# Kernel optimization log

Measured on AMD Instinct MI355X. Metric: run time of the kernel, lower is better.

Reference implementation:

```python
import jax, jax.numpy as jnp
import numpy as np

P = 16  # patch size
D = 768  # embedding dim


def setup_inputs() -> dict:
    key = jax.random.key(0)
    k_img, k_w, k_b = jax.random.split(key, 3)
    B, H, W, C = 64, 224, 224, 3
    image = jax.random.normal(k_img, (B, H, W, C), dtype=jnp.float32)
    patch_dim = P * P * C  # 768
    # Keras Dense default: glorot_uniform kernel, zeros bias
    limit = np.sqrt(6.0 / (patch_dim + D)).astype(np.float32)
    W_proj = jax.random.uniform(k_w, (patch_dim, D), dtype=jnp.float32,
                                minval=-limit, maxval=limit)
    b_proj = jnp.zeros((D,), dtype=jnp.float32)
    return {"image": image, "W_proj": W_proj, "b_proj": b_proj}


def reference(image, W_proj, b_proj):
    B, H, W, C = image.shape
    nh, nw = H // P, W // P
    # Fused im2col replacing the per-patch slicing loop:
    # [B,H,W,C] -> [B, nh, P, nw, P, C] -> [B, nh, nw, P, P, C] -> [B, nh*nw, P*P*C]
    # Row-major (p_i, p_j) patch order matches the original nested loop, and
    # flatten of a [B,P,P,C] slice matches the (P,P,C) raveling here.
    patches = image.reshape(B, nh, P, nw, P, C)
    patches = patches.transpose(0, 1, 3, 2, 4, 5).reshape(B, nh * nw, P * P * C)
    # Dense + exact GELU (tf.keras.activations.gelu default approximate=False)
    x = jnp.einsum('bnp,pd->bnd', patches, W_proj) + b_proj
    return jax.nn.gelu(x, approximate=False)
```

## Files before the change

kernel.cpp:

```cpp
#include <hip/hip_runtime.h>
#include <hip/hip_bf16.h>
#include <math.h>

#define MM 12544
#define KK 768
#define NN 768
#define BM 64
#define BN 128
#define BK 64
#define KT 12
#define MT 196
#define NT 6
#define TILE_B_BYTES (BN*BK*2)

#define WTPACK_BLOCKS ((NN * 96) / 256)

typedef __bf16 v8bf __attribute__((ext_vector_type(8)));
typedef float  v4f  __attribute__((ext_vector_type(4)));

__global__ __launch_bounds__(256) void wt_pack(const float* __restrict__ w,
                                               __hip_bfloat16* __restrict__ wpack) {
    int tid = blockIdx.x * 256 + threadIdx.x;
    int n   = tid % 768;
    int gg  = tid / 768;
    int k0  = gg * 8;
    float f[8];
#pragma unroll
    for (int j = 0; j < 8; j++) f[j] = w[(size_t)(k0 + j) * NN + n];
    int nt = n >> 7;
    int nr = n & 127;
    int kt = gg >> 3;
    int g  = gg & 7;
    int gs = g ^ (nr & 7);
    union { __hip_bfloat16 h[8]; uint4 u; } o;
#pragma unroll
    for (int j = 0; j < 8; j++) o.h[j] = __float2bfloat16(f[j]);
    *(uint4*)(wpack + ((size_t)(nt * KT + kt) * BN + nr) * BK + gs * 8) = o.u;
}

__device__ __forceinline__ float gelu_fast(float x) {
    float t2 = 1.5957691216057308f * x * (1.0f + 0.044715f * x * x);
    float e  = __expf(t2);
    float r  = __builtin_amdgcn_rcpf(e + 1.0f);
    return x - x * r;
}

__global__ __launch_bounds__(256, 5) void gemm_gelu(const float* __restrict__ img,
                                                    const __hip_bfloat16* __restrict__ wpack,
                                                    const float* __restrict__ bias,
                                                    float* __restrict__ out) {
    __shared__ __align__(16) __hip_bfloat16 As[BM * BK];
    __shared__ __align__(16) __hip_bfloat16 Bs[BN * BK];

    const int blk = blockIdx.x;
    const int nt  = blk % NT;
    const int mt  = blk / NT;

    const int tid  = threadIdx.x;
    const int lane = tid & 63;
    const int wave = tid >> 6;
    const int wn   = wave * 32;
    const int col  = lane & 15;
    const int quad = lane >> 4;
    const int cl7  = col & 7;

    const int r = tid >> 2;
    const int q = tid & 3;
    unsigned m  = (unsigned)(mt * BM + r);
    unsigned b  = m / 196u;
    unsigned pm = m - b * 196u;
    unsigned pr = pm / 14u;
    unsigned pc = pm - pr * 14u;
    const float* pbase = img + (size_t)(((b * 224u + pr * 16u) * 224u + pc * 16u) * 3u);
    const int gs0 = (2 * q) ^ (r & 7);
    const int gs1 = gs0 ^ 1;
    uint4* As16 = (uint4*)As;

    v4f acc[4][2];
    const v4f vzero = {0.f, 0.f, 0.f, 0.f};
#pragma unroll
    for (int a = 0; a < 4; a++)
#pragma unroll
        for (int c = 0; c < 2; c++) acc[a][c] = vzero;

    const char* bT = (const char*)wpack + (size_t)nt * KT * TILE_B_BYTES;

    for (int kt = 0; kt < KT; kt++) {
#pragma unroll
        for (int p = 0; p < 4; p++) {
            int off = p * 4096 + tid * 16;
            __builtin_amdgcn_global_load_lds(
                (const __attribute__((address_space(1))) void*)(bT + off),
                (__attribute__((address_space(3))) void*)((char*)Bs + off), 16, 0, 0);
        }
        bT += TILE_B_BYTES;

        float4 f4[4];
#pragma unroll
        for (int j = 0; j < 4; j++) {
            unsigned k   = (unsigned)(kt * 64 + q * 16 + j * 4);
            unsigned i   = k / 48u;
            unsigned rem = k - i * 48u;
            f4[j] = *(const float4*)(pbase + i * 672u + rem);
        }
        union { __hip_bfloat16 h[8]; uint4 u; } lo, hi;
        lo.h[0] = __float2bfloat16(f4[0].x); lo.h[1] = __float2bfloat16(f4[0].y);
        lo.h[2] = __float2bfloat16(f4[0].z); lo.h[3] = __float2bfloat16(f4[0].w);
        lo.h[4] = __float2bfloat16(f4[1].x); lo.h[5] = __float2bfloat16(f4[1].y);
        lo.h[6] = __float2bfloat16(f4[1].z); lo.h[7] = __float2bfloat16(f4[1].w);
        hi.h[0] = __float2bfloat16(f4[2].x); hi.h[1] = __float2bfloat16(f4[2].y);
        hi.h[2] = __float2bfloat16(f4[2].z); hi.h[3] = __float2bfloat16(f4[2].w);
        hi.h[4] = __float2bfloat16(f4[3].x); hi.h[5] = __float2bfloat16(f4[3].y);
        hi.h[6] = __float2bfloat16(f4[3].z); hi.h[7] = __float2bfloat16(f4[3].w);
        As16[r * 8 + gs0] = lo.u;
        As16[r * 8 + gs1] = hi.u;

        __syncthreads();

#pragma unroll
        for (int ks = 0; ks < 2; ks++) {
            const int gs = (ks * 4 + quad) ^ cl7;
            const v8bf* pa = (const v8bf*)(As + col * BK + gs * 8);
            const v8bf* pb = (const v8bf*)(Bs + (wn + col) * BK + gs * 8);
            v8bf af[4], bfr[2];
#pragma unroll
            for (int mi = 0; mi < 4; mi++) af[mi] = pa[mi * 128];
#pragma unroll
            for (int ni = 0; ni < 2; ni++) bfr[ni] = pb[ni * 128];
#pragma unroll
            for (int mi = 0; mi < 4; mi++)
#pragma unroll
                for (int ni = 0; ni < 2; ni++)
                    acc[mi][ni] = __builtin_amdgcn_mfma_f32_16x16x32_bf16(
                        af[mi], bfr[ni], acc[mi][ni], 0, 0, 0);
        }
        __syncthreads();
    }

#pragma unroll
    for (int ni = 0; ni < 2; ni++) {
        int n    = nt * BN + wn + ni * 16 + col;
        float bv = bias[n];
#pragma unroll
        for (int mi = 0; mi < 4; mi++) {
            int rowb = mt * BM + mi * 16 + quad * 4;
            float* po = out + (size_t)rowb * NN + n;
#pragma unroll
            for (int rg = 0; rg < 4; rg++) {
                float x = acc[mi][ni][rg] + bv;
                po[(size_t)rg * NN] = gelu_fast(x);
            }
        }
    }
}

extern "C" void kernel_launch(void* const* d_in, const int* in_sizes, int n_in,
                              void* d_out, int out_size, void* d_ws, size_t ws_size,
                              hipStream_t stream) {
    const float* img   = (const float*)d_in[0];
    const float* wproj = (const float*)d_in[1];
    const float* bias  = (const float*)d_in[2];
    float* out = (float*)d_out;

    __hip_bfloat16* wpack = (__hip_bfloat16*)d_ws;

    wt_pack<<<dim3(WTPACK_BLOCKS), dim3(256), 0, stream>>>(wproj, wpack);
    gemm_gelu<<<dim3(MT * NT), dim3(256), 0, stream>>>(img, wpack, bias, out);
}
```

Before: 131.2 us.

## Replace LDS-tiled GEMM with single-wave full-N register-accumulator kernel

Each single-wave block now computes 16 rows across all 768 output columns, holding 48 MFMA accumulators in registers. The A fragment is loaded straight from the image with register prefetch and the B fragments are read directly from a fragment-packed weight layout in global memory. Shared memory and barriers are gone, and the image is read only once instead of once per N-tile. In exchange the weights are re-read from L2 by every wave, register pressure rises sharply, and occupancy and latency hiding may suffer.

Result: slower. 353.5 us (+169.5%).

```diff
diff --git a/kernel.cpp b/kernel.cpp
--- a/kernel.cpp
+++ b/kernel.cpp
@@ -5,15 +5,9 @@
 #define MM 12544
 #define KK 768
 #define NN 768
-#define BM 64
-#define BN 128
-#define BK 64
-#define KT 12
-#define MT 196
-#define NT 6
-#define TILE_B_BYTES (BN*BK*2)
-
-#define WTPACK_BLOCKS ((NN * 96) / 256)
+#define KS 24
+#define NF 48
+#define NWAVES (MM / 16)
 
 typedef __bf16 v8bf __attribute__((ext_vector_type(8)));
 typedef float  v4f  __attribute__((ext_vector_type(4)));
@@ -21,21 +15,18 @@
 __global__ __launch_bounds__(256) void wt_pack(const float* __restrict__ w,
                                                __hip_bfloat16* __restrict__ wpack) {
     int tid = blockIdx.x * 256 + threadIdx.x;
-    int n   = tid % 768;
-    int gg  = tid / 768;
-    int k0  = gg * 8;
+    int l   = tid & 63;
+    int ft  = (tid >> 6) % NF;
+    int s   = (tid >> 6) / NF;
+    int n   = ft * 16 + (l & 15);
+    int k   = s * 32 + (l >> 4) * 8;
     float f[8];
 #pragma unroll
-    for (int j = 0; j < 8; j++) f[j] = w[(size_t)(k0 + j) * NN + n];
-    int nt = n >> 7;
-    int nr = n & 127;
-    int kt = gg >> 3;
-    int g  = gg & 7;
-    int gs = g ^ (nr & 7);
+    for (int j = 0; j < 8; j++) f[j] = w[(size_t)(k + j) * NN + n];
     union { __hip_bfloat16 h[8]; uint4 u; } o;
 #pragma unroll
     for (int j = 0; j < 8; j++) o.h[j] = __float2bfloat16(f[j]);
-    *(uint4*)(wpack + ((size_t)(nt * KT + kt) * BN + nr) * BK + gs * 8) = o.u;
+    *(uint4*)(wpack + (size_t)tid * 8) = o.u;
 }
 
 __device__ __forceinline__ float gelu_fast(float x) {
@@ -45,111 +36,71 @@
     return x - x * r;
 }
 
-__global__ __launch_bounds__(256, 5) void gemm_gelu(const float* __restrict__ img,
-                                                    const __hip_bfloat16* __restrict__ wpack,
-                                                    const float* __restrict__ bias,
-                                                    float* __restrict__ out) {
-    __shared__ __align__(16) __hip_bfloat16 As[BM * BK];
-    __shared__ __align__(16) __hip_bfloat16 Bs[BN * BK];
-
-    const int blk = blockIdx.x;
-    const int nt  = blk % NT;
-    const int mt  = blk / NT;
-
-    const int tid  = threadIdx.x;
-    const int lane = tid & 63;
-    const int wave = tid >> 6;
-    const int wn   = wave * 32;
+__global__ __launch_bounds__(64, 1) void gemm_gelu(const float* __restrict__ img,
+                                                   const __hip_bfloat16* __restrict__ wpack,
+                                                   const float* __restrict__ bias,
+                                                   float* __restrict__ out) {
+    const int wid  = blockIdx.x;
+    const int lane = threadIdx.x;
     const int col  = lane & 15;
     const int quad = lane >> 4;
-    const int cl7  = col & 7;
 
-    const int r = tid >> 2;
-    const int q = tid & 3;
-    unsigned m  = (unsigned)(mt * BM + r);
+    unsigned m  = (unsigned)(wid * 16 + col);
     unsigned b  = m / 196u;
     unsigned pm = m - b * 196u;
     unsigned pr = pm / 14u;
     unsigned pc = pm - pr * 14u;
     const float* pbase = img + (size_t)(((b * 224u + pr * 16u) * 224u + pc * 16u) * 3u);
-    const int gs0 = (2 * q) ^ (r & 7);
-    const int gs1 = gs0 ^ 1;
-    uint4* As16 = (uint4*)As;
 
-    v4f acc[4][2];
+    v4f acc[NF];
     const v4f vzero = {0.f, 0.f, 0.f, 0.f};
 #pragma unroll
-    for (int a = 0; a < 4; a++)
-#pragma unroll
-        for (int c = 0; c < 2; c++) acc[a][c] = vzero;
+    for (int t = 0; t < NF; t++) acc[t] = vzero;
 
-    const char* bT = (const char*)wpack + (size_t)nt * KT * TILE_B_BYTES;
-
-    for (int kt = 0; kt < KT; kt++) {
-#pragma unroll
-        for (int p = 0; p < 4; p++) {
-            int off = p * 4096 + tid * 16;
-            __builtin_amdgcn_global_load_lds(
-                (const __attribute__((address_space(1))) void*)(bT + off),
-                (__attribute__((address_space(3))) void*)((char*)Bs + off), 16, 0, 0);
-        }
-        bT += TILE_B_BYTES;
-
-        float4 f4[4];
-#pragma unroll
-        for (int j = 0; j < 4; j++) {
-            unsigned k   = (unsigned)(kt * 64 + q * 16 + j * 4);
-            unsigned i   = k / 48u;
-            unsigned rem = k - i * 48u;
-            f4[j] = *(const float4*)(pbase + i * 672u + rem);
-        }
-        union { __hip_bfloat16 h[8]; uint4 u; } lo, hi;
-        lo.h[0] = __float2bfloat16(f4[0].x); lo.h[1] = __float2bfloat16(f4[0].y);
-        lo.h[2] = __float2bfloat16(f4[0].z); lo.h[3] = __float2bfloat16(f4[0].w);
-        lo.h[4] = __float2bfloat16(f4[1].x); lo.h[5] = __float2bfloat16(f4[1].y);
-        lo.h[6] = __float2bfloat16(f4[1].z); lo.h[7] = __float2bfloat16(f4[1].w);
-        hi.h[0] = __float2bfloat16(f4[2].x); hi.h[1] = __float2bfloat16(f4[2].y);
-        hi.h[2] = __float2bfloat16(f4[2].z); hi.h[3] = __float2bfloat16(f4[2].w);
-        hi.h[4] = __float2bfloat16(f4[3].x); hi.h[5] = __float2bfloat16(f4[3].y);
-        hi.h[6] = __float2bfloat16(f4[3].z); hi.h[7] = __float2bfloat16(f4[3].w);
-        As16[r * 8 + gs0] = lo.u;
-        As16[r * 8 + gs1] = hi.u;
-
-        __syncthreads();
-
-#pragma unroll
-        for (int ks = 0; ks < 2; ks++) {
-            const int gs = (ks * 4 + quad) ^ cl7;
-            const v8bf* pa = (const v8bf*)(As + col * BK + gs * 8);
-            const v8bf* pb = (const v8bf*)(Bs + (wn + col) * BK + gs * 8);
-            v8bf af[4], bfr[2];
-#pragma unroll
-            for (int mi = 0; mi < 4; mi++) af[mi] = pa[mi * 128];
-#pragma unroll
-            for (int ni = 0; ni < 2; ni++) bfr[ni] = pb[ni * 128];
-#pragma unroll
-            for (int mi = 0; mi < 4; mi++)
-#pragma unroll
-                for (int ni = 0; ni < 2; ni++)
-                    acc[mi][ni] = __builtin_amdgcn_mfma_f32_16x16x32_bf16(
-                        af[mi], bfr[ni], acc[mi][ni], 0, 0, 0);
-        }
-        __syncthreads();
+    float4 c0, c1;
+    {
+        unsigned u   = (unsigned)quad;
+        unsigned i   = u / 6u;
+        unsigned rem = (u - i * 6u) * 8u;
+        const float* p = pbase + i * 672u + rem;
+        c0 = *(const float4*)p;
+        c1 = *(const float4*)(p + 4);
     }
 
+    const char* wl = (const char*)wpack + (size_t)lane * 16;
+
+    for (int s = 0; s < KS; s++) {
+        union { __hip_bfloat16 h[8]; v8bf v; } af;
+        af.h[0] = __float2bfloat16(c0.x); af.h[1] = __float2bfloat16(c0.y);
+        af.h[2] = __float2bfloat16(c0.z); af.h[3] = __float2bfloat16(c0.w);
+        af.h[4] = __float2bfloat16(c1.x); af.h[5] = __float2bfloat16(c1.y);
+        af.h[6] = __float2bfloat16(c1.z); af.h[7] = __float2bfloat16(c1.w);
+
+        if (s + 1 < KS) {
+            unsigned u   = (unsigned)(4 * (s + 1) + quad);
+            unsigned i   = u / 6u;
+            unsigned rem = (u - i * 6u) * 8u;
+            const float* p = pbase + i * 672u + rem;
+            c0 = *(const float4*)p;
+            c1 = *(const float4*)(p + 4);
+        }
+
+        const char* wf = wl + (size_t)s * NF * 1024;
 #pragma unroll
-    for (int ni = 0; ni < 2; ni++) {
-        int n    = nt * BN + wn + ni * 16 + col;
-        float bv = bias[n];
+        for (int t = 0; t < NF; t++) {
+            v8bf bf = *(const v8bf*)(wf + (size_t)t * 1024);
+            acc[t] = __builtin_amdgcn_mfma_f32_16x16x32_bf16(af.v, bf, acc[t], 0, 0, 0);
+        }
+    }
+
+    float* orow = out + ((size_t)(wid * 16 + quad * 4)) * NN + col;
 #pragma unroll
-        for (int mi = 0; mi < 4; mi++) {
-            int rowb = mt * BM + mi * 16 + quad * 4;
-            float* po = out + (size_t)rowb * NN + n;
+    for (int t = 0; t < NF; t++) {
+        float bv = bias[t * 16 + col];
 #pragma unroll
-            for (int rg = 0; rg < 4; rg++) {
-                float x = acc[mi][ni][rg] + bv;
-                po[(size_t)rg * NN] = gelu_fast(x);
-            }
+        for (int rg = 0; rg < 4; rg++) {
+            float x = acc[t][rg] + bv;
+            orow[(size_t)rg * NN + t * 16] = gelu_fast(x);
         }
     }
 }
@@ -164,6 +115,6 @@
 
     __hip_bfloat16* wpack = (__hip_bfloat16*)d_ws;
 
-    wt_pack<<<dim3(WTPACK_BLOCKS), dim3(256), 0, stream>>>(wproj, wpack);
-    gemm_gelu<<<dim3(MT * NT), dim3(256), 0, stream>>>(img, wpack, bias, out);
+    wt_pack<<<dim3((KS * NF * 64) / 256), dim3(256), 0, stream>>>(wproj, wpack);
+    gemm_gelu<<<dim3(NWAVES), dim3(64), 0, stream>>>(img, wpack, bias, out);
 }
```
